# Kernel optimization log

Measured on AMD Instinct MI355X. Metric: run time of the kernel, lower is better.

## Reference

```python
import jax, jax.numpy as jnp
import numpy as np

B, S, D, H = 1, 2048, 768, 12
HD = D // H


def layer_norm(x, g, b, eps=1e-5):
    mu = x.mean(-1, keepdims=True)
    var = ((x - mu) ** 2).mean(-1, keepdims=True)
    return (x - mu) * jax.lax.rsqrt(var + eps) * g + b


def setup_inputs() -> dict:
    key = jax.random.key(0)
    ks = jax.random.split(key, 16)
    s = 0.02
    exp_encodings = jax.random.normal(ks[0], (B, S, D), dtype=jnp.float32)
    pert_encodings = jax.random.normal(ks[1], (B, S, D), dtype=jnp.float32)
    adj = (jax.random.uniform(ks[2], (S, S)) < 0.01).astype(jnp.int32)
    adj = adj.at[jnp.arange(S), jnp.arange(S)].set(1)
    in_proj_w = jax.random.normal(ks[3], (3 * D, D)) * s
    in_proj_b = jnp.zeros((3 * D,), jnp.float32)
    out_proj_w = jax.random.normal(ks[4], (D, D)) * s
    out_proj_b = jnp.zeros((D,), jnp.float32)
    ln0_g = jnp.ones((D,), jnp.float32); ln0_b = jnp.zeros((D,), jnp.float32)
    ln1_g = jnp.ones((D,), jnp.float32); ln1_b = jnp.zeros((D,), jnp.float32)
    ln2_g = jnp.ones((D,), jnp.float32); ln2_b = jnp.zeros((D,), jnp.float32)
    w1 = jax.random.normal(ks[5], (D // 2, D)) * s
    b1 = jnp.zeros((D // 2,), jnp.float32)
    w2 = jax.random.normal(ks[6], (D, D // 2)) * s
    b2 = jnp.zeros((D,), jnp.float32)
    return dict(exp_encodings=exp_encodings, pert_encodings=pert_encodings,
                in_proj_w=in_proj_w, in_proj_b=in_proj_b,
                out_proj_w=out_proj_w, out_proj_b=out_proj_b,
                ln0_g=ln0_g, ln0_b=ln0_b, ln1_g=ln1_g, ln1_b=ln1_b,
                ln2_g=ln2_g, ln2_b=ln2_b, w1=w1, b1=b1, w2=w2, b2=b2,
                adj=adj)


def reference(exp_encodings, pert_encodings, in_proj_w, in_proj_b,
              out_proj_w, out_proj_b, ln0_g, ln0_b, ln1_g, ln1_b,
              ln2_g, ln2_b, w1, b1, w2, b2, adj):
    b, s, d = exp_encodings.shape
    hd = d // H
    # additive mask: 0 where edge, -inf elsewhere (diag guaranteed edge)
    mask = jnp.where(adj > 0, 0.0, -jnp.inf).astype(exp_encodings.dtype)
    x_in = layer_norm(exp_encodings + pert_encodings, ln0_g, ln0_b)
    # torch MultiheadAttention (batch_first) self-attention
    qkv = x_in @ in_proj_w.T + in_proj_b          # [b,s,3d]
    q, k, v = jnp.split(qkv, 3, axis=-1)
    q = q.reshape(b, s, H, hd)
    k = k.reshape(b, s, H, hd)
    v = v.reshape(b, s, H, hd)
    scores = jnp.einsum('bqhe,bkhe->bhqk', q, k) / np.sqrt(hd) + mask
    attn = jax.nn.softmax(scores, axis=-1)
    o = jnp.einsum('bhqk,bkhe->bqhe', attn, v).reshape(b, s, d)
    o = o @ out_proj_w.T + out_proj_b
    x = layer_norm(o + x_in, ln1_g, ln1_b)
    ff = jax.nn.relu(x @ w1.T + b1) @ w2.T + b2
    return layer_norm(x + ff, ln2_g, ln2_b)
```

## Files before the change

kernel.cpp:

```cpp
#include <hip/hip_runtime.h>

#define S 2048
#define D 768
#define NH 12
#define HD 64
#define TD (3 * D)

typedef __bf16 bf16_t;
typedef __bf16 v8bf __attribute__((ext_vector_type(8)));
typedef __bf16 v4bf __attribute__((ext_vector_type(4)));
typedef float v4f __attribute__((ext_vector_type(4)));

__device__ __forceinline__ float wave_reduce_sum(float v) {
#pragma unroll
    for (int o = 32; o > 0; o >>= 1) v += __shfl_down(v, o, 64);
    return v;
}
__device__ float block_reduce_sum(float v) {
    __shared__ float t4[4];
    int lane = threadIdx.x & 63, wid = threadIdx.x >> 6;
    v = wave_reduce_sum(v);
    __syncthreads();
    if (lane == 0) t4[wid] = v;
    __syncthreads();
    return t4[0] + t4[1] + t4[2] + t4[3];
}

#define NW0 (TD * D / 4)
#define NW1 (D * D / 4)
#define NW2 ((D / 2) * D / 4)
#define NW3 (D * (D / 2) / 4)
#define NWALL (NW0 + NW1 + NW2 + NW3)

__global__ __launch_bounds__(256) void addln_cvt(const float* __restrict__ A, const float* __restrict__ Bv,
                                                 const float* __restrict__ g, const float* __restrict__ be,
                                                 bf16_t* __restrict__ out,
                                                 const float* __restrict__ s0, const float* __restrict__ s1,
                                                 const float* __restrict__ s2, const float* __restrict__ s3,
                                                 bf16_t* __restrict__ d0, bf16_t* __restrict__ d1,
                                                 bf16_t* __restrict__ d2, bf16_t* __restrict__ d3) {
    int blk = blockIdx.x, t = threadIdx.x;
    if (blk >= S) {
        int i = (blk - S) * 256 + t;
        const float* sp; bf16_t* dp;
        if (i < NW0) { sp = s0; dp = d0; }
        else if (i < NW0 + NW1) { sp = s1; dp = d1; i -= NW0; }
        else if (i < NW0 + NW1 + NW2) { sp = s2; dp = d2; i -= NW0 + NW1; }
        else if (i < NWALL) { sp = s3; dp = d3; i -= NW0 + NW1 + NW2; }
        else return;
        float4 v = ((const float4*)sp)[i];
        v4bf o = {(bf16_t)v.x, (bf16_t)v.y, (bf16_t)v.z, (bf16_t)v.w};
        *(v4bf*)(dp + (size_t)i * 4) = o;
        return;
    }
    int row = blk;
    const float* a = A + (size_t)row * D;
    const float* b = Bv + (size_t)row * D;
    float x[3];
    float s = 0.f;
#pragma unroll
    for (int i = 0; i < 3; ++i) { int c = t + 256 * i; x[i] = a[c] + b[c]; s += x[i]; }
    float mean = block_reduce_sum(s) * (1.0f / D);
    float vs = 0.f;
#pragma unroll
    for (int i = 0; i < 3; ++i) { float d = x[i] - mean; vs += d * d; }
    float var = block_reduce_sum(vs) * (1.0f / D);
    float rstd = rsqrtf(var + 1e-5f);
#pragma unroll
    for (int i = 0; i < 3; ++i) {
        int c = t + 256 * i;
        out[(size_t)row * D + c] = (bf16_t)((x[i] - mean) * rstd * g[c] + be[c]);
    }
}

template <typename TO>
__global__ __launch_bounds__(256) void ln_only(const bf16_t* __restrict__ X,
                                               const float* __restrict__ g, const float* __restrict__ be,
                                               TO* __restrict__ out) {
    int row = blockIdx.x, t = threadIdx.x;
    const bf16_t* a = X + (size_t)row * D;
    float x[3];
    float s = 0.f;
#pragma unroll
    for (int i = 0; i < 3; ++i) { int c = t + 256 * i; x[i] = (float)a[c]; s += x[i]; }
    float mean = block_reduce_sum(s) * (1.0f / D);
    float vs = 0.f;
#pragma unroll
    for (int i = 0; i < 3; ++i) { float d = x[i] - mean; vs += d * d; }
    float var = block_reduce_sum(vs) * (1.0f / D);
    float rstd = rsqrtf(var + 1e-5f);
#pragma unroll
    for (int i = 0; i < 3; ++i) {
        int c = t + 256 * i;
        out[(size_t)row * D + c] = (TO)((x[i] - mean) * rstd * g[c] + be[c]);
    }
}

#define GBK 64

template <int TM, int TN, int RELU, bool RESID>
__global__ __launch_bounds__(256) void gemm_mfma(const bf16_t* __restrict__ A, const bf16_t* __restrict__ B,
                                                 const float* __restrict__ bias,
                                                 const bf16_t* __restrict__ Rsd, bf16_t* __restrict__ C,
                                                 int M, int N, int K) {
    constexpr int CA = TM * 8;
    constexpr int CHUNKS = (TM + TN) * 8;
    constexpr int P = CHUNKS / 256;
    static_assert(CHUNKS % 256 == 0, "chunk passes must be exact");
    constexpr int MI = TM / 32, NI = TN / 32;
    __shared__ bf16_t As[TM * GBK];
    __shared__ bf16_t Bs[TN * GBK];
    const int t = threadIdx.x;
    const int lane = t & 63, wave = t >> 6;
    const int wr = (wave >> 1) * (TM / 2), wc = (wave & 1) * (TN / 2);
    const int m0 = blockIdx.y * TM, n0 = blockIdx.x * TN;
    const int lm = lane & 15, q = lane >> 4;

    const bf16_t* gsrc[P];
    bf16_t* ldst[P];
#pragma unroll
    for (int p = 0; p < P; ++p) {
        int c = t + 256 * p;
        if (c < CA) {
            int slab = c / (TM * 4), r4 = c % (TM * 4);
            int row = r4 >> 2, c4 = r4 & 3;
            gsrc[p] = A + (size_t)(m0 + row) * K + slab * 32 + c4 * 8;
            ldst[p] = As + slab * (TM * 32) + row * 32 + c4 * 8;
        } else {
            int cc = c - CA;
            int slab = cc / (TN * 4), r4 = cc % (TN * 4);
            int row = r4 >> 2, c4 = r4 & 3;
            gsrc[p] = B + (size_t)(n0 + row) * K + slab * 32 + c4 * 8;
            ldst[p] = Bs + slab * (TN * 32) + row * 32 + c4 * 8;
        }
    }

    v4f acc[MI][NI] = {};

    for (int k0 = 0; k0 < K; k0 += GBK) {
#pragma unroll
        for (int p = 0; p < P; ++p)
            __builtin_amdgcn_global_load_lds((const __attribute__((address_space(1))) void*)(gsrc[p] + k0),
                                             (__attribute__((address_space(3))) void*)ldst[p], 16, 0, 0);
        __syncthreads();

        v8bf af[2][MI], bfr[2][NI];
#pragma unroll
        for (int s = 0; s < 2; ++s) {
#pragma unroll
            for (int i = 0; i < MI; ++i)
                af[s][i] = *(const v8bf*)(As + s * (TM * 32) + (wr + i * 16 + lm) * 32 + q * 8);
#pragma unroll
            for (int j = 0; j < NI; ++j)
                bfr[s][j] = *(const v8bf*)(Bs + s * (TN * 32) + (wc + j * 16 + lm) * 32 + q * 8);
        }
#pragma unroll
        for (int s = 0; s < 2; ++s)
#pragma unroll
            for (int i = 0; i < MI; ++i)
#pragma unroll
                for (int j = 0; j < NI; ++j)
                    acc[i][j] = __builtin_amdgcn_mfma_f32_16x16x32_bf16(af[s][i], bfr[s][j], acc[i][j], 0, 0, 0);
        __syncthreads();
    }

#pragma unroll
    for (int i = 0; i < MI; ++i)
#pragma unroll
        for (int j = 0; j < NI; ++j) {
            int col = n0 + wc + j * 16 + lm;
            float bs = bias[col];
#pragma unroll
            for (int r = 0; r < 4; ++r) {
                int row = m0 + wr + i * 16 + q * 4 + r;
                float v = acc[i][j][r] + bs;
                if (RELU) v = fmaxf(v, 0.f);
                if (RESID) v += (float)Rsd[(size_t)row * N + col];
                C[(size_t)row * N + col] = (bf16_t)v;
            }
        }
}

__global__ __launch_bounds__(256) void attn_sparse(const bf16_t* __restrict__ qkv, const int* __restrict__ adj,
                                                   bf16_t* __restrict__ O) {
    __shared__ int s_idx[128];
    __shared__ int s_cnt;
    __shared__ float s_q[D];
    __shared__ float s_p[NH][128];

    const int row = blockIdx.x, t = threadIdx.x;
    const int lane = t & 63, wave = t >> 6;
    if (t == 0) s_cnt = 0;
    __syncthreads();

    const int4* arow = (const int4*)(adj + (size_t)row * S);
#pragma unroll
    for (int p = 0; p < 2; ++p) {
        int4 v = arow[t + 256 * p];
        int base = (t + 256 * p) * 4;
        if (v.x) { int k = atomicAdd(&s_cnt, 1); if (k < 128) s_idx[k] = base + 0; }
        if (v.y) { int k = atomicAdd(&s_cnt, 1); if (k < 128) s_idx[k] = base + 1; }
        if (v.z) { int k = atomicAdd(&s_cnt, 1); if (k < 128) s_idx[k] = base + 2; }
        if (v.w) { int k = atomicAdd(&s_cnt, 1); if (k < 128) s_idx[k] = base + 3; }
    }
    for (int c = t; c < D; c += 256) s_q[c] = (float)qkv[(size_t)row * TD + c];
    __syncthreads();
    const int n = (s_cnt < 128) ? s_cnt : 128;

    for (int it = t; it < n * NH; it += 256) {
        int h = it / n, i = it - h * n;
        int j = s_idx[i];
        const bf16_t* kp = qkv + (size_t)j * TD + D + h * HD;
        const float* qp = s_q + h * HD;
        float dot = 0.f;
#pragma unroll
        for (int c = 0; c < HD; c += 8) {
            v8bf kv = *(const v8bf*)(kp + c);
#pragma unroll
            for (int e = 0; e < 8; ++e) dot += qp[c + e] * (float)kv[e];
        }
        s_p[h][i] = dot * 0.125f;
    }
    __syncthreads();

    for (int h = wave; h < NH; h += 4) {
        float v0 = (lane < n) ? s_p[h][lane] : -1e30f;
        float v1 = (lane + 64 < n) ? s_p[h][lane + 64] : -1e30f;
        float m = fmaxf(v0, v1);
#pragma unroll
        for (int o = 32; o > 0; o >>= 1) m = fmaxf(m, __shfl_xor(m, o, 64));
        float p0 = (lane < n) ? __expf(v0 - m) : 0.f;
        float p1 = (lane + 64 < n) ? __expf(v1 - m) : 0.f;
        float sm = p0 + p1;
#pragma unroll
        for (int o = 32; o > 0; o >>= 1) sm += __shfl_xor(sm, o, 64);
        float inv = 1.f / sm;
        if (lane < n) s_p[h][lane] = p0 * inv;
        if (lane + 64 < n) s_p[h][lane + 64] = p1 * inv;
    }
    __syncthreads();

    for (int o = t; o < D; o += 256) {
        int h = o >> 6, e = o & 63;
        const float* pp = s_p[h];
        float acc = 0.f;
        for (int i = 0; i < n; ++i)
            acc += pp[i] * (float)qkv[(size_t)s_idx[i] * TD + 2 * D + h * HD + e];
        O[(size_t)row * D + o] = (bf16_t)acc;
    }
}

extern "C" void kernel_launch(void* const* d_in, const int* in_sizes, int n_in,
                              void* d_out, int out_size, void* d_ws, size_t ws_size,
                              hipStream_t stream) {
    const float* exp_e = (const float*)d_in[0];
    const float* pert  = (const float*)d_in[1];
    const float* w_in  = (const float*)d_in[2];
    const float* b_in  = (const float*)d_in[3];
    const float* w_out = (const float*)d_in[4];
    const float* b_out = (const float*)d_in[5];
    const float* g0  = (const float*)d_in[6];
    const float* be0 = (const float*)d_in[7];
    const float* g1  = (const float*)d_in[8];
    const float* be1 = (const float*)d_in[9];
    const float* g2  = (const float*)d_in[10];
    const float* be2 = (const float*)d_in[11];
    const float* w1  = (const float*)d_in[12];
    const float* b1  = (const float*)d_in[13];
    const float* w2  = (const float*)d_in[14];
    const float* b2  = (const float*)d_in[15];
    const int*   adj = (const int*)d_in[16];
    float* out = (float*)d_out;

    const size_t SD = (size_t)S * D;
    bf16_t* wb_in  = (bf16_t*)d_ws;
    bf16_t* wb_out = wb_in + (size_t)TD * D;
    bf16_t* wb_1   = wb_out + (size_t)D * D;
    bf16_t* wb_2   = wb_1 + (size_t)(D / 2) * D;
    bf16_t* x_in   = wb_2 + (size_t)D * (D / 2);
    bf16_t* qkv    = x_in + SD;
    bf16_t* attn_o = qkv + 3 * SD;
    bf16_t* y1     = attn_o + SD;
    bf16_t* x1     = y1 + SD;
    bf16_t* ffh    = x1 + SD;
    bf16_t* y2     = ffh + SD / 2;

    const int CVTB = (NWALL + 255) / 256;
    addln_cvt<<<S + CVTB, 256, 0, stream>>>(exp_e, pert, g0, be0, x_in,
                                            w_in, w_out, w1, w2, wb_in, wb_out, wb_1, wb_2);
    gemm_mfma<64, 128, 0, false><<<dim3(TD / 128, S / 64), 256, 0, stream>>>(x_in, wb_in, b_in, nullptr, qkv, S, TD, D);
    attn_sparse<<<S, 256, 0, stream>>>(qkv, adj, attn_o);
    gemm_mfma<64, 64, 0, true><<<dim3(D / 64, S / 64), 256, 0, stream>>>(attn_o, wb_out, b_out, x_in, y1, S, D, D);
    ln_only<bf16_t><<<S, 256, 0, stream>>>(y1, g1, be1, x1);
    gemm_mfma<32, 64, 1, false><<<dim3((D / 2) / 64, S / 32), 256, 0, stream>>>(x1, wb_1, b1, nullptr, ffh, S, D / 2, D);
    gemm_mfma<64, 64, 0, true><<<dim3(D / 64, S / 64), 256, 0, stream>>>(ffh, wb_2, b2, x1, y2, S, D, D / 2);
    ln_only<float><<<S, 256, 0, stream>>>(y2, g2, be2, out);
}
```

Baseline: 196.0 us.

## Double-buffer GEMM LDS tiles with async prefetch of next K slab

Converts the MFMA GEMM mainloop to a double-buffered scheme: the next K tile is issued via global_load_lds into the alternate LDS buffer before computing on the current one, with explicit vmcnt waits and scheduling barriers. This aims to overlap global memory latency with MFMA compute instead of stalling on each tile load. It doubles LDS usage, which may reduce occupancy, and relies on hand-written waitcnt ordering being correct.

```diff
diff --git a/kernel.cpp b/kernel.cpp
--- a/kernel.cpp
+++ b/kernel.cpp
@@ -24,6 +24,19 @@
     if (lane == 0) t4[wid] = v;
     __syncthreads();
     return t4[0] + t4[1] + t4[2] + t4[3];
+}
+
+template <int N>
+__device__ __forceinline__ void wait_vmcnt() {
+    if constexpr (N == 0) asm volatile("s_waitcnt vmcnt(0)" ::: "memory");
+    else if constexpr (N == 1) asm volatile("s_waitcnt vmcnt(1)" ::: "memory");
+    else if constexpr (N == 2) asm volatile("s_waitcnt vmcnt(2)" ::: "memory");
+    else if constexpr (N == 3) asm volatile("s_waitcnt vmcnt(3)" ::: "memory");
+    else if constexpr (N == 4) asm volatile("s_waitcnt vmcnt(4)" ::: "memory");
+    else if constexpr (N == 5) asm volatile("s_waitcnt vmcnt(5)" ::: "memory");
+    else if constexpr (N == 6) asm volatile("s_waitcnt vmcnt(6)" ::: "memory");
+    else if constexpr (N == 7) asm volatile("s_waitcnt vmcnt(7)" ::: "memory");
+    else asm volatile("s_waitcnt vmcnt(8)" ::: "memory");
 }
 
 #define NW0 (TD * D / 4)
@@ -108,42 +121,57 @@
     constexpr int P = CHUNKS / 256;
     static_assert(CHUNKS % 256 == 0, "chunk passes must be exact");
     constexpr int MI = TM / 32, NI = TN / 32;
-    __shared__ bf16_t As[TM * GBK];
-    __shared__ bf16_t Bs[TN * GBK];
+    constexpr int BUFE = (TM + TN) * GBK;
+    __shared__ bf16_t smem[2 * BUFE];
     const int t = threadIdx.x;
     const int lane = t & 63, wave = t >> 6;
     const int wr = (wave >> 1) * (TM / 2), wc = (wave & 1) * (TN / 2);
     const int m0 = blockIdx.y * TM, n0 = blockIdx.x * TN;
     const int lm = lane & 15, q = lane >> 4;
 
-    const bf16_t* gsrc[P];
-    bf16_t* ldst[P];
+    const bf16_t* gp[P];
+    int loff[P];
 #pragma unroll
     for (int p = 0; p < P; ++p) {
         int c = t + 256 * p;
         if (c < CA) {
             int slab = c / (TM * 4), r4 = c % (TM * 4);
-            int row = r4 >> 2, c4 = r4 & 3;
-            gsrc[p] = A + (size_t)(m0 + row) * K + slab * 32 + c4 * 8;
-            ldst[p] = As + slab * (TM * 32) + row * 32 + c4 * 8;
+            gp[p] = A + (size_t)(m0 + (r4 >> 2)) * K + slab * 32 + (r4 & 3) * 8;
+            loff[p] = slab * (TM * 32) + r4 * 8;
         } else {
             int cc = c - CA;
             int slab = cc / (TN * 4), r4 = cc % (TN * 4);
-            int row = r4 >> 2, c4 = r4 & 3;
-            gsrc[p] = B + (size_t)(n0 + row) * K + slab * 32 + c4 * 8;
-            ldst[p] = Bs + slab * (TN * 32) + row * 32 + c4 * 8;
+            gp[p] = B + (size_t)(n0 + (r4 >> 2)) * K + slab * 32 + (r4 & 3) * 8;
+            loff[p] = TM * GBK + slab * (TN * 32) + r4 * 8;
         }
     }
 
     v4f acc[MI][NI] = {};
 
+    auto stage = [&](int buf, int k0) {
+#pragma unroll
+        for (int p = 0; p < P; ++p)
+            __builtin_amdgcn_global_load_lds(
+                (const __attribute__((address_space(1))) void*)(gp[p] + k0),
+                (__attribute__((address_space(3))) void*)(smem + buf * BUFE + loff[p]), 16, 0, 0);
+    };
+
+    stage(0, 0);
+    int cur = 0;
     for (int k0 = 0; k0 < K; k0 += GBK) {
-#pragma unroll
-        for (int p = 0; p < P; ++p)
-            __builtin_amdgcn_global_load_lds((const __attribute__((address_space(1))) void*)(gsrc[p] + k0),
-                                             (__attribute__((address_space(3))) void*)ldst[p], 16, 0, 0);
-        __syncthreads();
-
+        if (k0 + GBK < K) {
+            stage(cur ^ 1, k0 + GBK);
+            __builtin_amdgcn_sched_barrier(0);
+            wait_vmcnt<P>();
+        } else {
+            __builtin_amdgcn_sched_barrier(0);
+            wait_vmcnt<0>();
+        }
+        __builtin_amdgcn_s_barrier();
+        __builtin_amdgcn_sched_barrier(0);
+
+        const bf16_t* As = smem + cur * BUFE;
+        const bf16_t* Bs = As + TM * GBK;
         v8bf af[2][MI], bfr[2][NI];
 #pragma unroll
         for (int s = 0; s < 2; ++s) {
@@ -161,7 +189,9 @@
 #pragma unroll
                 for (int j = 0; j < NI; ++j)
                     acc[i][j] = __builtin_amdgcn_mfma_f32_16x16x32_bf16(af[s][i], bfr[s][j], acc[i][j], 0, 0, 0);
-        __syncthreads();
+        __builtin_amdgcn_sched_barrier(0);
+        __builtin_amdgcn_s_barrier();
+        cur ^= 1;
     }
 
 #pragma unroll
```

After: 188.7 us. 3.8% less time.
